# Kernel optimization log

Hardware: AMD Instinct MI355X
Metric: run time of the kernel (lower is better)

## Reference

```python
import jax, jax.numpy as jnp
import numpy as np

B, T, D = 4, 2048, 1024
H, HD = 16, 64  # num_heads, head_size


def setup_inputs() -> dict:
    key = jax.random.key(0)
    ks = jax.random.split(key, 6)
    x = jax.random.normal(ks[0], (B, T, D), dtype=jnp.float32)
    s = 1.0 / np.sqrt(D)
    Wq = jax.random.normal(ks[1], (H, D, HD), dtype=jnp.float32) * s
    Wk = jax.random.normal(ks[2], (H, D, HD), dtype=jnp.float32) * s
    Wv = jax.random.normal(ks[3], (H, D, HD), dtype=jnp.float32) * s
    Wp = jax.random.normal(ks[4], (H * HD, D), dtype=jnp.float32) * (1.0 / np.sqrt(H * HD))
    bp = jnp.zeros((D,), dtype=jnp.float32)
    return {"x": x, "Wq": Wq, "Wk": Wk, "Wv": Wv, "Wp": Wp, "bp": bp}


def reference(x, Wq, Wk, Wv, Wp, bp):
    # Per-head bias-free projections, batched over heads.
    q = jnp.einsum("btd,hde->bhte", x, Wq)  # [B,H,T,HD]
    k = jnp.einsum("btd,hde->bhte", x, Wk)
    v = jnp.einsum("btd,hde->bhte", x, Wv)
    scale = 1.0 / jnp.sqrt(jnp.asarray(HD, dtype=x.dtype))
    scores = jnp.einsum("bhte,bhse->bhts", q, k) * scale  # [B,H,T,T]
    causal = jnp.tril(jnp.ones((T, T), dtype=bool))
    scores = jnp.where(causal, scores, jnp.finfo(x.dtype).min)
    att = jax.nn.softmax(scores, axis=-1)
    out = jnp.einsum("bhts,bhse->bhte", att, v)  # [B,H,T,HD]
    out = out.transpose(0, 2, 1, 3).reshape(B, T, H * HD)  # concat heads
    return out @ Wp + bp  # [B,T,D] (dropout = identity in eval)
```

## Files before the change

### kernel.cpp

```cpp
#include <hip/hip_runtime.h>
#include <hip/hip_bf16.h>

#define B_  4
#define T_  2048
#define D_  1024
#define H_  16
#define HD_ 64
#define M_  (B_ * T_)
#define BH_ (B_ * H_)

typedef __attribute__((ext_vector_type(8))) short   short8;
typedef __attribute__((ext_vector_type(4))) float   f32x4;
typedef __attribute__((ext_vector_type(4))) unsigned short us4v;

#define MFMA16(a, b, c) __builtin_amdgcn_mfma_f32_16x16x32_bf16((a), (b), (c), 0, 0, 0)

__device__ __forceinline__ unsigned short f2bf(float f) {
    union { float f; unsigned u; } v; v.f = f;
    unsigned r = v.u + 0x7fffu + ((v.u >> 16) & 1u);
    return (unsigned short)(r >> 16);
}

__device__ __forceinline__ float exp2_fast(float x) {
    float r; asm("v_exp_f32 %0, %1" : "=v"(r) : "v"(x)); return r;
}
__device__ __forceinline__ unsigned cvt_pk_bf16(float lo, float hi) {
    unsigned r; asm("v_cvt_pk_bf16_f32 %0, %1, %2" : "=v"(r) : "v"(lo), "v"(hi)); return r;
}

__device__ __forceinline__ void gl_lds16(const void* g, void* l) {
    __builtin_amdgcn_global_load_lds(
        (const __attribute__((address_space(1))) void*)g,
        (__attribute__((address_space(3))) void*)l, 16, 0, 0);
}

__global__ __launch_bounds__(256) void cvt_x(const float* __restrict__ x,
                                             unsigned short* __restrict__ xb, int n4) {
    int i = blockIdx.x * 256 + threadIdx.x;
    if (i < n4) {
        float4 v = ((const float4*)x)[i];
        us4v o;
        o[0] = f2bf(v.x); o[1] = f2bf(v.y); o[2] = f2bf(v.z); o[3] = f2bf(v.w);
        ((us4v*)xb)[i] = o;
    }
}

__global__ __launch_bounds__(256) void tcvt_qkv(
        const float* __restrict__ Wq, const float* __restrict__ Wk,
        const float* __restrict__ Wv, unsigned short* __restrict__ dst) {
    __shared__ float tile[64][65];
    int z = blockIdx.z;
    int sel = z >> 4, head = z & 15;
    const float* s = (sel == 0 ? Wq : (sel == 1 ? Wk : Wv)) + (size_t)head * D_ * HD_;
    int r0 = blockIdx.x * 64;
    int tid = threadIdx.x;
    #pragma unroll
    for (int i = 0; i < 4; ++i) {
        int idx4 = i * 256 + tid;
        int r = idx4 >> 4, c4 = (idx4 & 15) * 4;
        float4 v = *(const float4*)&s[(size_t)(r0 + r) * HD_ + c4];
        tile[r][c4 + 0] = v.x; tile[r][c4 + 1] = v.y;
        tile[r][c4 + 2] = v.z; tile[r][c4 + 3] = v.w;
    }
    __syncthreads();
    #pragma unroll
    for (int i = 0; i < 4; ++i) {
        int idx4 = i * 256 + tid;
        int c = idx4 >> 4, r4 = (idx4 & 15) * 4;
        us4v o;
        o[0] = f2bf(tile[r4 + 0][c]); o[1] = f2bf(tile[r4 + 1][c]);
        o[2] = f2bf(tile[r4 + 2][c]); o[3] = f2bf(tile[r4 + 3][c]);
        *(us4v*)&dst[(size_t)(sel * 1024 + head * 64 + c) * D_ + r0 + r4] = o;
    }
}

__global__ __launch_bounds__(256) void tcvt(const float* __restrict__ src,
                                            unsigned short* __restrict__ dst,
                                            int src_ld, long src_z_str,
                                            int dst_row_base, int dst_ld) {
    __shared__ float tile[64][65];
    const float* s = src + (size_t)blockIdx.z * src_z_str;
    int r0 = blockIdx.x * 64, c0 = blockIdx.y * 64;
    int tid = threadIdx.x;
    #pragma unroll
    for (int i = 0; i < 4; ++i) {
        int idx4 = i * 256 + tid;
        int r = idx4 >> 4, c4 = (idx4 & 15) * 4;
        float4 v = *(const float4*)&s[(size_t)(r0 + r) * src_ld + c0 + c4];
        tile[r][c4 + 0] = v.x; tile[r][c4 + 1] = v.y;
        tile[r][c4 + 2] = v.z; tile[r][c4 + 3] = v.w;
    }
    __syncthreads();
    #pragma unroll
    for (int i = 0; i < 4; ++i) {
        int idx4 = i * 256 + tid;
        int c = idx4 >> 4, r4 = (idx4 & 15) * 4;
        us4v o;
        o[0] = f2bf(tile[r4 + 0][c]); o[1] = f2bf(tile[r4 + 1][c]);
        o[2] = f2bf(tile[r4 + 2][c]); o[3] = f2bf(tile[r4 + 3][c]);
        *(us4v*)&dst[(size_t)(dst_row_base + blockIdx.z * 64 + c0 + c) * dst_ld + r0 + r4] = o;
    }
}

__device__ __forceinline__ void stage_ab(const unsigned short* __restrict__ A,
                                         const unsigned short* __restrict__ Bt,
                                         size_t m0, size_t n0, int k0,
                                         unsigned short* Asb, unsigned short* Bsb,
                                         int tid) {
    #pragma unroll
    for (int c = 0; c < 2; ++c) {
        int idx = c * 256 + tid;
        int row = idx >> 2, qp = idx & 3;
        int ql = qp ^ ((row >> 1) & 3);
        gl_lds16(A  + (m0 + row) * (size_t)D_ + k0 + ql * 8, Asb + idx * 8);
        gl_lds16(Bt + (n0 + row) * (size_t)D_ + k0 + ql * 8, Bsb + idx * 8);
    }
}

__global__ __launch_bounds__(256) void qkv_mfma(
        const unsigned short* __restrict__ A,
        const unsigned short* __restrict__ Bt,
        unsigned short* __restrict__ qb, unsigned short* __restrict__ kb,
        unsigned short* __restrict__ vT) {
    __shared__ unsigned short As[2][128 * 32];
    __shared__ unsigned short Bs[2][128 * 32];
    const int tid = threadIdx.x;
    const int lane = tid & 63, wid = tid >> 6;
    const int l16 = lane & 15, l4 = lane >> 4;
    const int wr = wid >> 1, wc = wid & 1;
    const int ksw = (l16 >> 1) & 3;

    const int orig = blockIdx.x;
    const int wgid = (orig & 7) * 192 + (orig >> 3);
    const size_t m0 = (size_t)(wgid / 24) * 128;
    const size_t n0 = (size_t)(wgid % 24) * 128;

    f32x4 acc[4][4] = {};
    stage_ab(A, Bt, m0, n0, 0, As[0], Bs[0], tid);
    asm volatile("s_waitcnt vmcnt(0)" ::: "memory");
    __syncthreads();

    for (int t = 0; t < 32; ++t) {
        const int cur = t & 1;
        if (t < 31)
            stage_ab(A, Bt, m0, n0, (t + 1) * 32, As[cur ^ 1], Bs[cur ^ 1], tid);
        const unsigned short* Ab = As[cur];
        const unsigned short* Bb = Bs[cur];
        short8 a[4], b[4];
        #pragma unroll
        for (int i = 0; i < 4; ++i)
            a[i] = *(const short8*)&Ab[(wr * 64 + i * 16 + l16) * 32 + ((l4 ^ ksw) * 8)];
        #pragma unroll
        for (int j = 0; j < 4; ++j)
            b[j] = *(const short8*)&Bb[(wc * 64 + j * 16 + l16) * 32 + ((l4 ^ ksw) * 8)];
        #pragma unroll
        for (int i = 0; i < 4; ++i)
            #pragma unroll
            for (int j = 0; j < 4; ++j)
                acc[i][j] = MFMA16(a[i], b[j], acc[i][j]);
        asm volatile("s_waitcnt vmcnt(0)" ::: "memory");
        __syncthreads();
    }

    #pragma unroll
    for (int j = 0; j < 4; ++j) {
        int n = (int)n0 + wc * 64 + j * 16 + l16;
        int sel = n >> 10, h = (n >> 6) & (H_ - 1), e = n & 63;
        if (sel == 2) {
            #pragma unroll
            for (int i = 0; i < 4; ++i) {
                int m = (int)m0 + wr * 64 + i * 16 + l4 * 4;
                int b_ = m >> 11, tt = m & (T_ - 1);
                us4v o;
                #pragma unroll
                for (int r = 0; r < 4; ++r) o[r] = f2bf(acc[i][j][r]);
                *(us4v*)&vT[((size_t)(b_ * H_ + h) * HD_ + e) * T_ + tt] = o;
            }
        } else {
            float scale = (sel == 0) ? 0.18033688011112042f : 1.0f;
            unsigned short* dst = (sel == 0) ? qb : kb;
            #pragma unroll
            for (int i = 0; i < 4; ++i) {
                #pragma unroll
                for (int r = 0; r < 4; ++r) {
                    int m = (int)m0 + wr * 64 + i * 16 + l4 * 4 + r;
                    int b_ = m >> 11, tt = m & (T_ - 1);
                    dst[((size_t)(b_ * H_ + h) * T_ + tt) * HD_ + e] = f2bf(acc[i][j][r] * scale);
                }
            }
        }
    }
}

__device__ __forceinline__ void stage_kv(const unsigned short* kbase,
                                         const unsigned short* vbase,
                                         unsigned short* KsBuf, unsigned short* VsBuf,
                                         int jt, int wid, int lane) {
    int s = lane & 7, rl = lane >> 3;
    int cchunk = s ^ rl;
    #pragma unroll
    for (int cc = 0; cc < 2; ++cc) {
        int chunk = cc * 4 + wid;
        int r = chunk * 8 + rl;
        gl_lds16(kbase + (size_t)(jt + r) * HD_ + cchunk * 8,
                 KsBuf + chunk * 512 + lane * 8);
        gl_lds16(vbase + (size_t)r * T_ + jt + cchunk * 8,
                 VsBuf + chunk * 512 + lane * 8);
    }
}

__device__ __forceinline__ void attn_tile_step(
        const unsigned short* Ksb, const unsigned short* Vsb, unsigned short* Pw,
        short8 qf0, short8 qf1, int diag, int wid, int l16, int l4,
        f32x4 (&o)[4], float& m, float& l) {
    f32x4 s[4];
    const int swz = l16 & 7;
    #pragma unroll
    for (int sc = 0; sc < 4; ++sc) {
        int row = sc * 16 + l16;
        int sl0 = l4 ^ swz;
        short8 kf0 = *(const short8*)&Ksb[row * 64 + sl0 * 8];
        short8 kf1 = *(const short8*)&Ksb[row * 64 + (sl0 ^ 4) * 8];
        f32x4 z = {0.f, 0.f, 0.f, 0.f};
        z = MFMA16(kf0, qf0, z);
        z = MFMA16(kf1, qf1, z);
        s[sc] = z;
    }
    if (diag) {
        int qloc = wid * 16 + l16;
        #pragma unroll
        for (int sc = 0; sc < 4; ++sc) {
            int kb0 = sc * 16 + l4 * 4;
            #pragma unroll
            for (int r = 0; r < 4; ++r)
                if (kb0 + r > qloc) s[sc][r] = -1e30f;
        }
    }
    float vmax = s[0][0];
    #pragma unroll
    for (int sc = 0; sc < 4; ++sc)
        #pragma unroll
        for (int r = 0; r < 4; ++r) vmax = fmaxf(vmax, s[sc][r]);
    vmax = fmaxf(vmax, __shfl_xor(vmax, 16));
    vmax = fmaxf(vmax, __shfl_xor(vmax, 32));

    if (!__all(vmax - m <= 8.0f)) {
        float mn = fmaxf(m, vmax);
        float corr = exp2_fast(m - mn);
        m = mn;
        l *= corr;
        #pragma unroll
        for (int r = 0; r < 4; ++r) {
            float cr = __shfl(corr, l4 * 4 + r);
            #pragma unroll
            for (int ec = 0; ec < 4; ++ec) o[ec][r] *= cr;
        }
    }
    float psum = 0.f;
    char* prow = (char*)Pw + l16 * 128;
    #pragma unroll
    for (int sc = 0; sc < 4; ++sc) {
        float p0 = exp2_fast(s[sc][0] - m);
        float p1 = exp2_fast(s[sc][1] - m);
        float p2 = exp2_fast(s[sc][2] - m);
        float p3 = exp2_fast(s[sc][3] - m);
        psum += (p0 + p1) + (p2 + p3);
        uint2 w;
        w.x = cvt_pk_bf16(p0, p1);
        w.y = cvt_pk_bf16(p2, p3);
        *(uint2*)(prow + ((sc * 32 + l4 * 8) ^ (swz << 4))) = w;
    }
    psum += __shfl_xor(psum, 16);
    psum += __shfl_xor(psum, 32);
    l += psum;

    asm volatile("s_waitcnt lgkmcnt(0)" ::: "memory");
    __builtin_amdgcn_sched_barrier(0);
    #pragma unroll
    for (int kc = 0; kc < 2; ++kc) {
        short8 pf = *(const short8*)(prow + ((kc * 64 + l4 * 16) ^ (swz << 4)));
        #pragma unroll
        for (int ec = 0; ec < 4; ++ec) {
            int vrow = ec * 16 + l16;
            int chunk = kc * 4 + l4;
            short8 vf = *(const short8*)&Vsb[vrow * 64 + ((chunk ^ swz) * 8)];
            o[ec] = MFMA16(pf, vf, o[ec]);
        }
    }
}

__global__ __launch_bounds__(256) void attn2(
        const unsigned short* __restrict__ qb, const unsigned short* __restrict__ kb,
        const unsigned short* __restrict__ vT, unsigned short* __restrict__ Ob) {
    __shared__ unsigned short Ks[2][64 * 64];
    __shared__ unsigned short Vs[2][64 * 64];
    __shared__ unsigned short Pl[4][16 * 64];

    const int blk = blockIdx.x;
    const int bh = (blk & 7) + 8 * ((blk >> 3) & 7);
    const int pair = blk >> 6;
    const int iA = pair, iB = 31 - pair;
    const int t0A = iA * 64, t0B = iB * 64;
    const int b = bh >> 4, h = bh & (H_ - 1);

    const int lane = threadIdx.x & 63, wid = threadIdx.x >> 6;
    const int l16 = lane & 15, l4 = lane >> 4;

    const unsigned short* kbase = kb + (size_t)bh * T_ * HD_;
    const unsigned short* vbase = vT + (size_t)bh * HD_ * T_;
    const unsigned short* qbase = qb + (size_t)bh * T_ * HD_;

    short8 qA0, qA1, qB0, qB1;
    {
        const unsigned short* qr = qbase + (size_t)(t0A + wid * 16 + l16) * HD_;
        qA0 = *(const short8*)(qr + l4 * 8);
        qA1 = *(const short8*)(qr + 32 + l4 * 8);
        qr = qbase + (size_t)(t0B + wid * 16 + l16) * HD_;
        qB0 = *(const short8*)(qr + l4 * 8);
        qB1 = *(const short8*)(qr + 32 + l4 * 8);
    }

    f32x4 oA[4] = {}, oB[4] = {};
    float mA = -__builtin_inff(), lA = 0.f;
    float mB = -__builtin_inff(), lB = 0.f;

    stage_kv(kbase, vbase, Ks[0], Vs[0], 0, wid, lane);
    asm volatile("s_waitcnt vmcnt(0)" ::: "memory");
    __syncthreads();

    for (int it = 0; it <= iB; ++it) {
        const int cur = it & 1;
        if (it < iB)
            stage_kv(kbase, vbase, Ks[cur ^ 1], Vs[cur ^ 1], (it + 1) * 64, wid, lane);
        if (it <= iA)
            attn_tile_step(Ks[cur], Vs[cur], Pl[wid], qA0, qA1, it == iA,
                           wid, l16, l4, oA, mA, lA);
        attn_tile_step(Ks[cur], Vs[cur], Pl[wid], qB0, qB1, it == iB,
                       wid, l16, l4, oB, mB, lB);
        asm volatile("s_waitcnt vmcnt(0)" ::: "memory");
        __syncthreads();
    }

    #pragma unroll
    for (int r = 0; r < 4; ++r) {
        float lr = __shfl(lA, l4 * 4 + r);
        float inv = 1.f / lr;
        int t = t0A + wid * 16 + l4 * 4 + r;
        unsigned short* orow = Ob + ((size_t)(b * T_ + t)) * D_ + h * HD_;
        #pragma unroll
        for (int ec = 0; ec < 4; ++ec)
            orow[ec * 16 + l16] = f2bf(oA[ec][r] * inv);
    }
    #pragma unroll
    for (int r = 0; r < 4; ++r) {
        float lr = __shfl(lB, l4 * 4 + r);
        float inv = 1.f / lr;
        int t = t0B + wid * 16 + l4 * 4 + r;
        unsigned short* orow = Ob + ((size_t)(b * T_ + t)) * D_ + h * HD_;
        #pragma unroll
        for (int ec = 0; ec < 4; ++ec)
            orow[ec * 16 + l16] = f2bf(oB[ec][r] * inv);
    }
}

__global__ __launch_bounds__(256) void proj_mfma(
        const unsigned short* __restrict__ A,
        const unsigned short* __restrict__ Bt,
        const float* __restrict__ bp, float* __restrict__ out) {
    __shared__ unsigned short As[2][128 * 32];
    __shared__ unsigned short Bs[2][128 * 32];
    const int tid = threadIdx.x;
    const int lane = tid & 63, wid = tid >> 6;
    const int l16 = lane & 15, l4 = lane >> 4;
    const int wr = wid >> 1, wc = wid & 1;
    const int ksw = (l16 >> 1) & 3;

    const int orig = blockIdx.x;
    const int wgid = (orig & 7) * 64 + (orig >> 3);
    const size_t m0 = (size_t)(wgid >> 3) * 128;
    const size_t n0 = (size_t)(wgid & 7) * 128;

    f32x4 acc[4][4] = {};
    stage_ab(A, Bt, m0, n0, 0, As[0], Bs[0], tid);
    asm volatile("s_waitcnt vmcnt(0)" ::: "memory");
    __syncthreads();

    for (int t = 0; t < 32; ++t) {
        const int cur = t & 1;
        if (t < 31)
            stage_ab(A, Bt, m0, n0, (t + 1) * 32, As[cur ^ 1], Bs[cur ^ 1], tid);
        const unsigned short* Ab = As[cur];
        const unsigned short* Bb = Bs[cur];
        short8 a[4], b[4];
        #pragma unroll
        for (int i = 0; i < 4; ++i)
            a[i] = *(const short8*)&Ab[(wr * 64 + i * 16 + l16) * 32 + ((l4 ^ ksw) * 8)];
        #pragma unroll
        for (int j = 0; j < 4; ++j)
            b[j] = *(const short8*)&Bb[(wc * 64 + j * 16 + l16) * 32 + ((l4 ^ ksw) * 8)];
        #pragma unroll
        for (int i = 0; i < 4; ++i)
            #pragma unroll
            for (int j = 0; j < 4; ++j)
                acc[i][j] = MFMA16(a[i], b[j], acc[i][j]);
        asm volatile("s_waitcnt vmcnt(0)" ::: "memory");
        __syncthreads();
    }

    #pragma unroll
    for (int j = 0; j < 4; ++j) {
        int n = (int)n0 + wc * 64 + j * 16 + l16;
        float bias = bp[n];
        #pragma unroll
        for (int i = 0; i < 4; ++i)
            #pragma unroll
            for (int r = 0; r < 4; ++r) {
                int m = (int)m0 + wr * 64 + i * 16 + l4 * 4 + r;
                out[(size_t)m * D_ + n] = acc[i][j][r] + bias;
            }
    }
}

extern "C" void kernel_launch(void* const* d_in, const int* in_sizes, int n_in,
                              void* d_out, int out_size, void* d_ws, size_t ws_size,
                              hipStream_t stream) {
    const float* x  = (const float*)d_in[0];
    const float* Wq = (const float*)d_in[1];
    const float* Wk = (const float*)d_in[2];
    const float* Wv = (const float*)d_in[3];
    const float* Wp = (const float*)d_in[4];
    const float* bp = (const float*)d_in[5];
    float* out = (float*)d_out;

    char* w = (char*)d_ws;
    unsigned short* xb  = (unsigned short*)w; w += (size_t)M_ * D_ * 2;
    unsigned short* Wt  = (unsigned short*)w; w += (size_t)3 * D_ * D_ * 2;
    unsigned short* Wpt = (unsigned short*)w; w += (size_t)D_ * D_ * 2;
    unsigned short* qb  = (unsigned short*)w; w += (size_t)BH_ * T_ * HD_ * 2;
    unsigned short* kb  = (unsigned short*)w; w += (size_t)BH_ * T_ * HD_ * 2;
    unsigned short* vT  = (unsigned short*)w; w += (size_t)BH_ * T_ * HD_ * 2;
    unsigned short* Ob  = (unsigned short*)w; w += (size_t)M_ * D_ * 2;

    cvt_x<<<dim3((M_ * D_ / 4 + 255) / 256), 256, 0, stream>>>(x, xb, M_ * D_ / 4);
    tcvt_qkv<<<dim3(16, 1, 48), 256, 0, stream>>>(Wq, Wk, Wv, Wt);
    tcvt<<<dim3(16, 16, 1), 256, 0, stream>>>(Wp, Wpt, D_, 0, 0, D_);

    qkv_mfma<<<dim3(1536), 256, 0, stream>>>(xb, Wt, qb, kb, vT);
    attn2<<<dim3(1024), 256, 0, stream>>>(qb, kb, vT, Ob);
    proj_mfma<<<dim3(512), 256, 0, stream>>>(Ob, Wpt, bp, out);
}
```

Before: 207.9 us.

## Replace LDS P round-trip with bpermute and interleave two attention tiles

Removes the per-wave LDS staging of the softmax probabilities and instead redistributes the packed bf16 P values between lanes with ds_bpermute, dropping the lgkmcnt wait and sched barrier. The loop is restructured so the QK MFMA of tile B is issued between softmax and PV of tile A, letting matrix and VALU/exp work overlap. It raises wave priority around MFMA bursts and sets launch_bounds occupancy hint to 4 blocks. This costs extra bpermute instructions and select ops, adds register pressure, and depends on the lane mapping being correct. In the interleaved path tile B's QK is called with diag=0, which is only safe when iA < iB.

```diff
diff --git a/kernel.cpp b/kernel.cpp
--- a/kernel.cpp
+++ b/kernel.cpp
@@ -26,6 +26,9 @@
 }
 __device__ __forceinline__ unsigned cvt_pk_bf16(float lo, float hi) {
     unsigned r; asm("v_cvt_pk_bf16_f32 %0, %1, %2" : "=v"(r) : "v"(lo), "v"(hi)); return r;
+}
+__device__ __forceinline__ int bperm(int addr, int src) {
+    return __builtin_amdgcn_ds_bpermute(addr, src);
 }
 
 __device__ __forceinline__ void gl_lds16(const void* g, void* l) {
@@ -209,12 +212,11 @@
     }
 }
 
-__device__ __forceinline__ void attn_tile_step(
-        const unsigned short* Ksb, const unsigned short* Vsb, unsigned short* Pw,
+__device__ __forceinline__ void qk_score(const unsigned short* Ksb,
         short8 qf0, short8 qf1, int diag, int wid, int l16, int l4,
-        f32x4 (&o)[4], float& m, float& l) {
-    f32x4 s[4];
+        f32x4 (&s)[4]) {
     const int swz = l16 & 7;
+    __builtin_amdgcn_s_setprio(1);
     #pragma unroll
     for (int sc = 0; sc < 4; ++sc) {
         int row = sc * 16 + l16;
@@ -226,6 +228,7 @@
         z = MFMA16(kf1, qf1, z);
         s[sc] = z;
     }
+    __builtin_amdgcn_s_setprio(0);
     if (diag) {
         int qloc = wid * 16 + l16;
         #pragma unroll
@@ -236,6 +239,11 @@
                 if (kb0 + r > qloc) s[sc][r] = -1e30f;
         }
     }
+}
+
+__device__ __forceinline__ void sm_pack(const f32x4 (&s)[4],
+        int l16, int l4, f32x4 (&o)[4], float& m, float& l,
+        unsigned (&W)[4][2]) {
     float vmax = s[0][0];
     #pragma unroll
     for (int sc = 0; sc < 4; ++sc)
@@ -257,7 +265,6 @@
         }
     }
     float psum = 0.f;
-    char* prow = (char*)Pw + l16 * 128;
     #pragma unroll
     for (int sc = 0; sc < 4; ++sc) {
         float p0 = exp2_fast(s[sc][0] - m);
@@ -265,20 +272,37 @@
         float p2 = exp2_fast(s[sc][2] - m);
         float p3 = exp2_fast(s[sc][3] - m);
         psum += (p0 + p1) + (p2 + p3);
-        uint2 w;
-        w.x = cvt_pk_bf16(p0, p1);
-        w.y = cvt_pk_bf16(p2, p3);
-        *(uint2*)(prow + ((sc * 32 + l4 * 8) ^ (swz << 4))) = w;
+        W[sc][0] = cvt_pk_bf16(p0, p1);
+        W[sc][1] = cvt_pk_bf16(p2, p3);
     }
     psum += __shfl_xor(psum, 16);
     psum += __shfl_xor(psum, 32);
     l += psum;
-
-    asm volatile("s_waitcnt lgkmcnt(0)" ::: "memory");
-    __builtin_amdgcn_sched_barrier(0);
+}
+
+__device__ __forceinline__ void pv_acc(const unsigned short* Vsb,
+        const unsigned (&W)[4][2], int l16, int l4, int addrLo, bool sel_lo,
+        f32x4 (&o)[4]) {
+    const int swz = l16 & 7;
+    const int addrHi = addrLo + 64;
     #pragma unroll
     for (int kc = 0; kc < 2; ++kc) {
-        short8 pf = *(const short8*)(prow + ((kc * 64 + l4 * 16) ^ (swz << 4)));
+        int b0, b1;
+        union { unsigned u[4]; short8 s; } pu;
+        b0 = bperm(addrLo, (int)W[kc * 2][0]);
+        b1 = bperm(addrLo, (int)W[kc * 2 + 1][0]);
+        pu.u[0] = sel_lo ? (unsigned)b0 : (unsigned)b1;
+        b0 = bperm(addrLo, (int)W[kc * 2][1]);
+        b1 = bperm(addrLo, (int)W[kc * 2 + 1][1]);
+        pu.u[1] = sel_lo ? (unsigned)b0 : (unsigned)b1;
+        b0 = bperm(addrHi, (int)W[kc * 2][0]);
+        b1 = bperm(addrHi, (int)W[kc * 2 + 1][0]);
+        pu.u[2] = sel_lo ? (unsigned)b0 : (unsigned)b1;
+        b0 = bperm(addrHi, (int)W[kc * 2][1]);
+        b1 = bperm(addrHi, (int)W[kc * 2 + 1][1]);
+        pu.u[3] = sel_lo ? (unsigned)b0 : (unsigned)b1;
+        short8 pf = pu.s;
+        __builtin_amdgcn_s_setprio(1);
         #pragma unroll
         for (int ec = 0; ec < 4; ++ec) {
             int vrow = ec * 16 + l16;
@@ -286,15 +310,15 @@
             short8 vf = *(const short8*)&Vsb[vrow * 64 + ((chunk ^ swz) * 8)];
             o[ec] = MFMA16(pf, vf, o[ec]);
         }
-    }
-}
-
-__global__ __launch_bounds__(256) void attn2(
+        __builtin_amdgcn_s_setprio(0);
+    }
+}
+
+__global__ __launch_bounds__(256, 4) void attn2(
         const unsigned short* __restrict__ qb, const unsigned short* __restrict__ kb,
         const unsigned short* __restrict__ vT, unsigned short* __restrict__ Ob) {
     __shared__ unsigned short Ks[2][64 * 64];
     __shared__ unsigned short Vs[2][64 * 64];
-    __shared__ unsigned short Pl[4][16 * 64];
 
     const int blk = blockIdx.x;
     const int bh = (blk & 7) + 8 * ((blk >> 3) & 7);
@@ -305,6 +329,8 @@
 
     const int lane = threadIdx.x & 63, wid = threadIdx.x >> 6;
     const int l16 = lane & 15, l4 = lane >> 4;
+    const int addrLo = ((2 * (l4 & 1)) * 16 + l16) * 4;
+    const bool sel_lo = (l4 < 2);
 
     const unsigned short* kbase = kb + (size_t)bh * T_ * HD_;
     const unsigned short* vbase = vT + (size_t)bh * HD_ * T_;
@@ -332,11 +358,26 @@
         const int cur = it & 1;
         if (it < iB)
             stage_kv(kbase, vbase, Ks[cur ^ 1], Vs[cur ^ 1], (it + 1) * 64, wid, lane);
-        if (it <= iA)
-            attn_tile_step(Ks[cur], Vs[cur], Pl[wid], qA0, qA1, it == iA,
-                           wid, l16, l4, oA, mA, lA);
-        attn_tile_step(Ks[cur], Vs[cur], Pl[wid], qB0, qB1, it == iB,
-                       wid, l16, l4, oB, mB, lB);
+        const unsigned short* Ksb = Ks[cur];
+        const unsigned short* Vsb = Vs[cur];
+        if (it <= iA) {
+            f32x4 sA[4];
+            qk_score(Ksb, qA0, qA1, it == iA, wid, l16, l4, sA);
+            unsigned WA[4][2];
+            sm_pack(sA, l16, l4, oA, mA, lA, WA);
+            f32x4 sB[4];
+            qk_score(Ksb, qB0, qB1, 0, wid, l16, l4, sB);
+            pv_acc(Vsb, WA, l16, l4, addrLo, sel_lo, oA);
+            unsigned WB[4][2];
+            sm_pack(sB, l16, l4, oB, mB, lB, WB);
+            pv_acc(Vsb, WB, l16, l4, addrLo, sel_lo, oB);
+        } else {
+            f32x4 sB[4];
+            qk_score(Ksb, qB0, qB1, it == iB, wid, l16, l4, sB);
+            unsigned WB[4][2];
+            sm_pack(sB, l16, l4, oB, mB, lB, WB);
+            pv_acc(Vsb, WB, l16, l4, addrLo, sel_lo, oB);
+        }
         asm volatile("s_waitcnt vmcnt(0)" ::: "memory");
         __syncthreads();
     }
```

After: 204.3 us. No clear change (-1.7%).
